# Optimization experiments

Hardware: AMD Instinct MI355X
Metric: run time of the kernel (lower is better)

Reference implementation:

```python
import jax, jax.numpy as jnp
import numpy as np

B, N, C = 4, 4096, 16
HID, OUT = 64, 64
ALL_K, K = 128, 32          # k + k_pos = 32
KD, KDP = 8, 6              # k_dilated, k_dilated_pos
EPS = 1e-5
NEG_SLOPE = 0.2


def setup_inputs() -> dict:
    ks = jax.random.split(jax.random.key(0), 12)
    C2, C4 = 2 * C, 4 * C
    return {
        "x": jax.random.normal(ks[0], (B, N, C), jnp.float32),
        "pos": jax.random.normal(ks[1], (B, N, 3), jnp.float32),
        "W1": jax.random.normal(ks[2], (C2, C2), jnp.float32) * 0.1,
        "g1": jnp.ones((C2,), jnp.float32),
        "b1": jnp.zeros((C2,), jnp.float32),
        "W2": jax.random.normal(ks[3], (HID, C4), jnp.float32) * 0.05,
        "g2": jnp.ones((HID,), jnp.float32),
        "b2": jnp.zeros((HID,), jnp.float32),
        "W3": jax.random.normal(ks[4], (OUT, HID), jnp.float32) * 0.05,
        "g3": jnp.ones((OUT,), jnp.float32),
        "b3": jnp.zeros((OUT,), jnp.float32),
    }


def pdist2(a):
    # squared pairwise distances (same top-k ordering as cdist p=2, and
    # avoids sqrt(0) on the diagonal). a: (B,N,D) -> (B,N,N)
    sq = jnp.sum(a * a, axis=-1)
    d = sq[:, :, None] + sq[:, None, :] - 2.0 * jnp.einsum('bnd,bmd->bnm', a, a)
    return jnp.maximum(d, 0.0)


def knn_excl_self(d2, k):
    # k nearest excluding self (self is the unique 0-distance nearest point)
    idx = jax.lax.top_k(-d2, k + 1)[1]
    return idx[..., 1:]


def fps(pts, npoint):
    # pts: (M, Kn, 3). Deterministic start at index 0 (torch version uses a
    # random start; only the sampled index set differs, math is identical).
    M, Kn, _ = pts.shape
    rows = jnp.arange(M)

    def body(i, state):
        centroids, distance, farthest = state
        centroids = centroids.at[:, i].set(farthest)
        centroid = pts[rows, farthest][:, None, :]            # (M,1,3)
        dist = jnp.sum((pts - centroid) ** 2, axis=-1)         # (M,Kn)
        distance = jnp.minimum(distance, dist)
        farthest = jnp.argmax(distance, axis=-1).astype(jnp.int32)
        return centroids, distance, farthest

    init = (jnp.zeros((M, npoint), jnp.int32),
            jnp.full((M, Kn), 1e10, jnp.float32),
            jnp.zeros((M,), jnp.int32))
    centroids, _, _ = jax.lax.fori_loop(0, npoint, body, init)
    return centroids


def edge_feat(feat, idx):
    # feat: (B,N,D) node features, idx: (B,N,Kn) neighbor indices
    # returns cat(neighbor - center, center): (B,N,Kn,2D)  (edge_function 249)
    nbr = feat[jnp.arange(feat.shape[0])[:, None, None], idx]  # (B,N,Kn,D)
    ctr = feat[:, :, None, :]
    return jnp.concatenate([nbr - ctr, jnp.broadcast_to(ctr, nbr.shape)], axis=-1)


def bn_lrelu(h, g, b):
    # BatchNorm2d with track_running_stats=False -> always batch stats.
    # h: (B,N,Kn,Cc), stats over (B,N,Kn) per channel.
    mu = jnp.mean(h, axis=(0, 1, 2), keepdims=True)
    var = jnp.var(h, axis=(0, 1, 2), keepdims=True)
    h = (h - mu) * jax.lax.rsqrt(var + EPS) * g + b
    return jnp.where(h > 0, h, NEG_SLOPE * h)


def reference(x, pos, W1, g1, b1, W2, g2, b2, W3, g3, b3):
    # --- dilated neighborhood: all_k nearest by position, FPS down to k ---
    cd2 = pdist2(pos)                                   # (B,N,N)
    idx_l = jax.lax.top_k(-cd2, ALL_K)[1]               # (B,N,ALL_K) incl. self
    idx_l_flat = idx_l.reshape(B * N, ALL_K)
    pts = pos.reshape(B * N, 3)[idx_l_flat]             # (B*N, ALL_K, 3)
    idx_fps_local = fps(pts, K)                         # (B*N, K)
    idx_fps = jnp.take_along_axis(idx_l_flat, idx_fps_local, axis=1)
    idx_fps = idx_fps.reshape(B, N, K)                  # (B,N,K)

    # --- dual kNN graph: k_dilated by feature distance + k_dilated_pos by pos ---
    idx_feat = knn_excl_self(pdist2(x), KD)             # (B,N,KD)
    idx_pos = knn_excl_self(cd2, KDP)                   # (B,N,KDP)
    idx1 = jnp.concatenate([idx_feat, idx_pos], axis=2)  # (B,N,KD+KDP)

    # --- conv1x1-BN-LeakyReLU on dual-graph edge features, max over nbrs ---
    e1 = edge_feat(x, idx1)                             # (B,N,14,2C)
    h1 = bn_lrelu(jnp.einsum('bnkc,oc->bnko', e1, W1), g1, b1)
    f1 = jnp.max(h1, axis=2)                            # (B,N,2C)

    # --- edge features on FPS-dilated graph, two conv1x1-BN-LeakyReLU ---
    e2 = edge_feat(f1, idx_fps)                         # (B,N,K,4C)
    h2 = bn_lrelu(jnp.einsum('bnkc,hc->bnkh', e2, W2), g2, b2)
    h3 = bn_lrelu(jnp.einsum('bnkh,oh->bnko', h2, W3), g3, b3)
    out = jnp.max(h3, axis=2)                           # (B,N,OUT)
    return out, idx1
```

## Files before the change

### kernel.cpp

```cpp
#include <hip/hip_runtime.h>

#define NPTS 4096
#define BNROWS 16384

__device__ __forceinline__ float lrelu(float h) { return h > 0.f ? h : 0.2f * h; }

__global__ __launch_bounds__(512) void knn_pos_kernel(
    const float* __restrict__ pos, int* __restrict__ idx_l,
    int* __restrict__ idx1_i, float* __restrict__ idx1_f)
{
  __shared__ unsigned long long cKey[8][512];
  __shared__ int cIdx[8][512];
  __shared__ unsigned int cCnt[8];
  int tid = threadIdx.x;
  int w = tid >> 6, lane = tid & 63;
  int r = blockIdx.x * 8 + w;
  int b = r >> 12, n = r & 4095;
  const float* pb = pos + (size_t)b * NPTS * 3;
  float cx = pb[n*3+0], cy = pb[n*3+1], cz = pb[n*3+2];
  if (lane == 0) cCnt[w] = 0u;

  unsigned int qp[32];
  int m1 = 65536, m2 = 65536, m3 = 65536;
  #pragma unroll
  for (int t = 0; t < 32; ++t) {
    unsigned int wq = 0u;
    #pragma unroll
    for (int h = 0; h < 2; ++h) {
      int j = (2*t + h) * 64 + lane;
      float dx = cx - pb[j*3+0], dy = cy - pb[j*3+1], dz = cz - pb[j*3+2];
      float d2 = dx*dx + dy*dy + dz*dz;
      int q = (int)(d2 * 1000.0f);
      q = q < 0 ? 0 : (q > 65535 ? 65535 : q);
      wq |= ((unsigned int)q) << (16*h);
      int nm1 = min(m1, q);
      int nm2 = min(m2, max(m1, q));
      int nm3 = min(m3, max(m2, q));
      m1 = nm1; m2 = nm2; m3 = nm3;
    }
    qp[t] = wq;
  }
  int lo = 0, hi = 65535;
  #pragma unroll
  for (int it = 0; it < 16; ++it) {
    int mid = (lo + hi) >> 1;
    int cnt = __popcll(__ballot(m3 <= mid));
    if (cnt >= 43) hi = mid; else lo = mid + 1;
  }
  unsigned int qt = (unsigned int)lo + 2u;

  #pragma unroll
  for (int t = 0; t < 32; ++t) {
    unsigned int wq = qp[t];
    unsigned int q0 = wq & 0xffffu, q1 = wq >> 16;
    if (q0 <= qt) { unsigned int p = atomicAdd(&cCnt[w], 1u); if (p < 512u) cIdx[w][p] = (2*t)*64 + lane; }
    if (q1 <= qt) { unsigned int p = atomicAdd(&cCnt[w], 1u); if (p < 512u) cIdx[w][p] = (2*t+1)*64 + lane; }
  }
  __syncthreads();
  unsigned int nc = cCnt[w]; if (nc > 512u) nc = 512u;

  double cxd = (double)cx, cyd = (double)cy, czd = (double)cz;
  #pragma unroll
  for (int t = 0; t < 8; ++t) {
    int c = lane + 64*t;
    unsigned long long kk = ~0ull; int id = 0x7fffffff;
    if (c < (int)nc) {
      id = cIdx[w][c];
      double dx = cxd - (double)pb[id*3+0];
      double dy = cyd - (double)pb[id*3+1];
      double dz = czd - (double)pb[id*3+2];
      kk = (unsigned long long)__double_as_longlong(dx*dx + dy*dy + dz*dz);
    }
    cKey[w][c] = kk; cIdx[w][c] = id;
  }
  __syncthreads();

  for (int k = 2; k <= 512; k <<= 1) {
    for (int j = k >> 1; j > 0; j >>= 1) {
      #pragma unroll
      for (int t = 0; t < 8; ++t) {
        int i = lane + 64*t;
        int ixj = i ^ j;
        if (ixj > i) {
          unsigned long long ka = cKey[w][i], kb = cKey[w][ixj];
          int ia = cIdx[w][i], ib = cIdx[w][ixj];
          bool agtb = (ka > kb) || (ka == kb && ia > ib);
          bool up = ((i & k) == 0);
          if (agtb == up) { cKey[w][i] = kb; cKey[w][ixj] = ka; cIdx[w][i] = ib; cIdx[w][ixj] = ia; }
        }
      }
      __syncthreads();
    }
  }
  idx_l[(size_t)r * 128 + lane]      = cIdx[w][lane];
  idx_l[(size_t)r * 128 + lane + 64] = cIdx[w][lane + 64];
  if (lane < 6) {
    int v = cIdx[w][1 + lane];
    idx1_i[r * 14 + 8 + lane] = v;
    idx1_f[r * 14 + 8 + lane] = (float)v;
  }
}

__global__ __launch_bounds__(512) void knn_feat_kernel(
    const float* __restrict__ x, int* __restrict__ idx1_i, float* __restrict__ idx1_f)
{
  __shared__ float ctrf[8][16];
  __shared__ float4 cm2[8][5];
  __shared__ unsigned short lmin[8][512];
  __shared__ int cand[8][192];
  __shared__ unsigned int cCnt[8];
  __shared__ unsigned short qtS[8];
  int tid = threadIdx.x;
  int rbase = blockIdx.x * 8;
  int b = rbase >> 12;
  const float* xb = x + (size_t)b * NPTS * 16;

  if (tid < 128) {
    int rr = tid >> 4, c = tid & 15;
    float v = xb[(size_t)((rbase + rr) & 4095) * 16 + c];
    ctrf[rr][c] = v;
    ((float*)&cm2[rr][0])[c] = -2.0f * v;
  }
  if (tid < 8) cCnt[tid] = 0u;
  __syncthreads();
  if (tid < 8) {
    float s = 0.f;
    for (int c = 0; c < 16; ++c) { float v = ctrf[tid][c]; s += v * v; }
    cm2[tid][4].x = s;
  }
  __syncthreads();

  unsigned int qp[8][4];
  int minq[8];
  #pragma unroll
  for (int r = 0; r < 8; ++r) minq[r] = 65536;

  #pragma unroll
  for (int pp = 0; pp < 4; ++pp) {
    int j0 = tid + 512 * (2*pp);
    int j1 = j0 + 512;
    const float4* xj0 = (const float4*)(xb + (size_t)j0 * 16);
    const float4* xj1 = (const float4*)(xb + (size_t)j1 * 16);
    float4 a0 = xj0[0], a1 = xj0[1], a2 = xj0[2], a3 = xj0[3];
    float4 b0 = xj1[0], b1 = xj1[1], b2 = xj1[2], b3 = xj1[3];
    float va[16] = {a0.x,a0.y,a0.z,a0.w, a1.x,a1.y,a1.z,a1.w,
                    a2.x,a2.y,a2.z,a2.w, a3.x,a3.y,a3.z,a3.w};
    float vb[16] = {b0.x,b0.y,b0.z,b0.w, b1.x,b1.y,b1.z,b1.w,
                    b2.x,b2.y,b2.z,b2.w, b3.x,b3.y,b3.z,b3.w};
    float pna = 0.f, pnb = 0.f;
    #pragma unroll
    for (int c = 0; c < 16; ++c) { pna = fmaf(va[c], va[c], pna); pnb = fmaf(vb[c], vb[c], pnb); }
    #pragma unroll
    for (int r = 0; r < 8; ++r) {
      float4 m0 = cm2[r][0], m1 = cm2[r][1], m2 = cm2[r][2], m3 = cm2[r][3];
      float c2 = cm2[r][4].x;
      float wm[16] = {m0.x,m0.y,m0.z,m0.w, m1.x,m1.y,m1.z,m1.w,
                      m2.x,m2.y,m2.z,m2.w, m3.x,m3.y,m3.z,m3.w};
      float aa = pna + c2, ab = pnb + c2;
      #pragma unroll
      for (int c = 0; c < 16; ++c) { aa = fmaf(wm[c], va[c], aa); ab = fmaf(wm[c], vb[c], ab); }
      int qa = (int)(aa * 400.0f); qa = qa < 0 ? 0 : (qa > 65535 ? 65535 : qa);
      int qb = (int)(ab * 400.0f); qb = qb < 0 ? 0 : (qb > 65535 ? 65535 : qb);
      qp[r][pp] = (unsigned int)qa | ((unsigned int)qb << 16);
      minq[r] = min(minq[r], min(qa, qb));
    }
  }
  #pragma unroll
  for (int r = 0; r < 8; ++r) lmin[r][tid] = (unsigned short)minq[r];
  __syncthreads();

  int w = tid >> 6, lane = tid & 63;
  {
    unsigned short lv[8];
    #pragma unroll
    for (int t = 0; t < 8; ++t) lv[t] = lmin[w][lane + 64*t];
    int lo = 0, hi = 65535;
    #pragma unroll
    for (int it = 0; it < 16; ++it) {
      int mid = (lo + hi) >> 1;
      int cnt = 0;
      #pragma unroll
      for (int t = 0; t < 8; ++t) cnt += __popcll(__ballot((int)lv[t] <= mid));
      if (cnt >= 10) hi = mid; else lo = mid + 1;
    }
    if (lane == 0) qtS[w] = (unsigned short)min(lo + 2, 65535);
  }
  __syncthreads();

  {
    unsigned int qts[8];
    #pragma unroll
    for (int r = 0; r < 8; ++r) qts[r] = qtS[r];
    #pragma unroll
    for (int r = 0; r < 8; ++r) {
      #pragma unroll
      for (int pp = 0; pp < 4; ++pp) {
        unsigned int wq = qp[r][pp];
        unsigned int q0 = wq & 0xffffu, q1 = wq >> 16;
        if (q0 <= qts[r]) { unsigned int p = atomicAdd(&cCnt[r], 1u); if (p < 192u) cand[r][p] = tid + 512*(2*pp); }
        if (q1 <= qts[r]) { unsigned int p = atomicAdd(&cCnt[r], 1u); if (p < 192u) cand[r][p] = tid + 512*(2*pp+1); }
      }
    }
  }
  __syncthreads();

  {
    int nc = (int)cCnt[w]; if (nc > 192) nc = 192;
    double key[3]; int kid[3];
    #pragma unroll
    for (int s = 0; s < 3; ++s) {
      int c = lane + 64*s;
      if (c < nc) {
        int id = cand[w][c];
        const float4* xp = (const float4*)(xb + (size_t)id * 16);
        float4 q0 = xp[0], q1 = xp[1], q2 = xp[2], q3 = xp[3];
        float xv[16] = {q0.x,q0.y,q0.z,q0.w, q1.x,q1.y,q1.z,q1.w,
                        q2.x,q2.y,q2.z,q2.w, q3.x,q3.y,q3.z,q3.w};
        double acc = 0.0;
        #pragma unroll
        for (int c2 = 0; c2 < 16; ++c2) { double d = (double)ctrf[w][c2] - (double)xv[c2]; acc += d * d; }
        key[s] = acc; kid[s] = id;
      } else { key[s] = 1e300; kid[s] = 0x7fffffff; }
    }
    int row = rbase + w;
    for (int it = 0; it < 9; ++it) {
      double bk = key[0]; int bi = kid[0], bs = 0;
      if (key[1] < bk || (key[1] == bk && kid[1] < bi)) { bk = key[1]; bi = kid[1]; bs = 1; }
      if (key[2] < bk || (key[2] == bk && kid[2] < bi)) { bk = key[2]; bi = kid[2]; bs = 2; }
      double rk = bk; int ri = bi;
      #pragma unroll
      for (int off = 32; off > 0; off >>= 1) {
        double ok = __shfl_xor(rk, off, 64);
        int oi = __shfl_xor(ri, off, 64);
        if (ok < rk || (ok == rk && oi < ri)) { rk = ok; ri = oi; }
      }
      if (it > 0 && lane == 0) {
        idx1_i[row * 14 + it - 1] = ri;
        idx1_f[row * 14 + it - 1] = (float)ri;
      }
      if (bi == ri) key[bs] = 1e300;
    }
  }
}

__global__ __launch_bounds__(256) void fps_kernel(
    const float* __restrict__ pos, const int* __restrict__ idx_l, int* __restrict__ idx_fps)
{
  int wave = threadIdx.x >> 6, lane = threadIdx.x & 63;
  int r = blockIdx.x * 4 + wave;
  const int* il = idx_l + (size_t)r * 128;
  int gi0 = il[lane], gi1 = il[lane + 64];
  double x0 = (double)pos[gi0*3+0], y0 = (double)pos[gi0*3+1], z0 = (double)pos[gi0*3+2];
  double x1 = (double)pos[gi1*3+0], y1 = (double)pos[gi1*3+1], z1 = (double)pos[gi1*3+2];
  double d0 = 1e10, d1 = 1e10;
  int far = 0;
  int* outp = idx_fps + (size_t)r * 32;
  for (int i = 0; i < 32; ++i) {
    int ownerLane = far & 63;
    int sel = far >> 6;
    int gsel = sel ? gi1 : gi0;
    int gout = __shfl(gsel, ownerLane, 64);
    if (lane == 0) outp[i] = gout;
    double cx = __shfl(sel ? x1 : x0, ownerLane, 64);
    double cy = __shfl(sel ? y1 : y0, ownerLane, 64);
    double cz = __shfl(sel ? z1 : z0, ownerLane, 64);
    double t0 = (x0-cx)*(x0-cx) + (y0-cy)*(y0-cy) + (z0-cz)*(z0-cz);
    double t1 = (x1-cx)*(x1-cx) + (y1-cy)*(y1-cy) + (z1-cz)*(z1-cz);
    d0 = fmin(d0, t0); d1 = fmin(d1, t1);
    double v; int p;
    if (d1 > d0) { v = d1; p = lane + 64; } else { v = d0; p = lane; }
    for (int off = 32; off > 0; off >>= 1) {
      double ov = __shfl_xor(v, off, 64);
      int op = __shfl_xor(p, off, 64);
      if (ov > v || (ov == v && op < p)) { v = ov; p = op; }
    }
    far = p;
  }
}

__global__ __launch_bounds__(256) void sv_kernel(
    const float* __restrict__ x, const float* __restrict__ W1,
    float* __restrict__ s, float* __restrict__ v)
{
  __shared__ float xs[8][16];
  __shared__ float w1t[512], w1dt[512];
  int tid = threadIdx.x;
  int rbase = blockIdx.x * 8;
  for (int i = tid; i < 512; i += 256) {
    int c = i >> 5, o = i & 31;
    float a = W1[o * 32 + c], bb = W1[o * 32 + 16 + c];
    w1t[i] = a; w1dt[i] = bb - a;
  }
  if (tid < 128) { int rr = tid >> 4, c = tid & 15; xs[rr][c] = x[(size_t)(rbase + rr) * 16 + c]; }
  __syncthreads();
  int rr = tid >> 5, o = tid & 31;
  float sa = 0.f, va = 0.f;
  #pragma unroll
  for (int c = 0; c < 16; ++c) {
    float xv = xs[rr][c];
    sa = fmaf(xv, w1t[c * 32 + o], sa);
    va = fmaf(xv, w1dt[c * 32 + o], va);
  }
  int r = rbase + rr;
  s[(size_t)r * 32 + o] = sa;
  v[(size_t)r * 32 + o] = va;
}

__global__ __launch_bounds__(256) void h1stats_kernel(
    const float* __restrict__ s, const float* __restrict__ v, const int* __restrict__ idx1_i,
    double* __restrict__ slotsH1, float* __restrict__ h1max)
{
  __shared__ int sidx[8][14];
  __shared__ float sred[256], sred2[256];
  int tid = threadIdx.x;
  int rr = tid >> 5, o = tid & 31;
  int rbase = blockIdx.x * 8;
  if (tid < 112) { int q = tid / 14, k = tid % 14; sidx[q][k] = idx1_i[(rbase + q) * 14 + k]; }
  __syncthreads();
  int r = rbase + rr;
  int broff = r & ~4095;
  float vv = v[(size_t)r * 32 + o];
  float m = -3.4e38f, ls = 0.f, lss = 0.f;
  #pragma unroll
  for (int k = 0; k < 14; ++k) {
    int j = sidx[rr][k];
    float val = s[(size_t)(broff + j) * 32 + o] + vv;
    m = fmaxf(m, val);
    ls += val; lss += val * val;
  }
  h1max[(size_t)r * 32 + o] = m;
  sred[tid] = ls; sred2[tid] = lss;
  __syncthreads();
  if (tid < 32) {
    float s2 = 0.f, ss = 0.f;
    #pragma unroll
    for (int j = 0; j < 8; ++j) { s2 += sred[j * 32 + tid]; ss += sred2[j * 32 + tid]; }
    int slot = blockIdx.x & 255;
    atomicAdd(&slotsH1[slot * 64 + tid], (double)s2);
    atomicAdd(&slotsH1[slot * 64 + 32 + tid], (double)ss);
  }
}

__global__ void finalize_stats_kernel(const double* __restrict__ slots, int C, double cnt,
    const float* __restrict__ g, const float* __restrict__ bta, float* __restrict__ scsh)
{
  int o = threadIdx.x;
  if (o < C) {
    double s = 0.0, ss = 0.0;
    for (int slot = 0; slot < 256; ++slot) { s += slots[slot * 2 * C + o]; ss += slots[slot * 2 * C + C + o]; }
    double mu = s / cnt;
    double var = ss / cnt - mu * mu;
    double rs = 1.0 / sqrt(var + 1e-5);
    float sc = (float)rs * g[o];
    float sh = bta[o] - (float)mu * sc;
    scsh[o] = sc;
    scsh[C + o] = sh;
  }
}

__global__ __launch_bounds__(256) void tu_kernel(
    const float* __restrict__ h1max, const float* __restrict__ scsh1, const float* __restrict__ W2,
    float* __restrict__ t, float* __restrict__ u)
{
  __shared__ float f1s[4][32];
  __shared__ float w2t[2048], w2dt[2048];
  int tid = threadIdx.x;
  int rbase = blockIdx.x * 4;
  for (int i = tid; i < 2048; i += 256) {
    int c = i >> 6, o = i & 63;
    float a = W2[o * 64 + c], bb = W2[o * 64 + 32 + c];
    w2t[i] = a; w2dt[i] = bb - a;
  }
  if (tid < 128) {
    int rr = tid >> 5, c = tid & 31;
    f1s[rr][c] = lrelu(h1max[(size_t)(rbase + rr) * 32 + c] * scsh1[c] + scsh1[32 + c]);
  }
  __syncthreads();
  int rr = tid >> 6, o = tid & 63;
  float ta = 0.f, ua = 0.f;
  #pragma unroll
  for (int c = 0; c < 32; ++c) {
    float fv = f1s[rr][c];
    ta = fmaf(fv, w2t[c * 64 + o], ta);
    ua = fmaf(fv, w2dt[c * 64 + o], ua);
  }
  int r = rbase + rr;
  t[(size_t)r * 64 + o] = ta;
  u[(size_t)r * 64 + o] = ua;
}

__global__ __launch_bounds__(256) void h2stats_kernel(
    const float* __restrict__ t, const float* __restrict__ u, const int* __restrict__ idx_fps,
    double* __restrict__ slotsH2)
{
  __shared__ int nids[8][32];
  __shared__ float sred[256], sred2[256];
  int tid = threadIdx.x;
  int o = tid & 63, wv = tid >> 6;
  int rbase = blockIdx.x * 8;
  { int q = tid >> 5, k = tid & 31; nids[q][k] = idx_fps[(rbase + q) * 32 + k]; }
  __syncthreads();
  float ls = 0.f, lss = 0.f;
  for (int rr = 0; rr < 8; ++rr) {
    int r = rbase + rr;
    int broff = r & ~4095;
    float uo = u[(size_t)r * 64 + o];
    #pragma unroll
    for (int i = 0; i < 8; ++i) {
      int k = wv + 4 * i;
      float val = t[(size_t)(broff + nids[rr][k]) * 64 + o] + uo;
      ls += val; lss += val * val;
    }
  }
  sred[tid] = ls; sred2[tid] = lss;
  __syncthreads();
  if (tid < 64) {
    float s2 = sred[tid] + sred[tid + 64] + sred[tid + 128] + sred[tid + 192];
    float ss = sred2[tid] + sred2[tid + 64] + sred2[tid + 128] + sred2[tid + 192];
    int slot = blockIdx.x & 255;
    atomicAdd(&slotsH2[slot * 128 + tid], (double)s2);
    atomicAdd(&slotsH2[slot * 128 + 64 + tid], (double)ss);
  }
}

#define ROWS3 8
__global__ __launch_bounds__(256, 4) void h3_kernel(
    const float* __restrict__ t, const float* __restrict__ u, const int* __restrict__ idx_fps,
    const float* __restrict__ W3, const float* __restrict__ scsh2,
    double* __restrict__ slotsH3, float* __restrict__ h3max)
{
  __shared__ float h2lds[2048];
  __shared__ float wmax[256];
  __shared__ float sred[256], sred2[256];
  __shared__ int nids[ROWS3][32];
  int tid = threadIdx.x;
  int o = tid & 63, wv = tid >> 6;
  float4 w3r[16];
  const float4* w3p = (const float4*)(W3 + o * 64);
  #pragma unroll
  for (int j = 0; j < 16; ++j) w3r[j] = w3p[j];
  float sc2o = scsh2[o], sh2o = scsh2[64 + o];
  int rbase = blockIdx.x * ROWS3;
  { int q = tid >> 5, k = tid & 31; nids[q][k] = idx_fps[(rbase + q) * 32 + k]; }
  float ls = 0.f, lss = 0.f;
  __syncthreads();
  for (int rr = 0; rr < ROWS3; ++rr) {
    int r = rbase + rr;
    int broff = r & ~4095;
    float uo = u[(size_t)r * 64 + o];
    #pragma unroll
    for (int i = 0; i < 8; ++i) {
      int k = wv + 4 * i;
      float val = t[(size_t)(broff + nids[rr][k]) * 64 + o] + uo;
      h2lds[k * 64 + o] = lrelu(val * sc2o + sh2o);
    }
    __syncthreads();
    float kmax = -3.4e38f;
    #pragma unroll
    for (int i = 0; i < 8; ++i) {
      int k = wv + 4 * i;
      const float4* hp = (const float4*)(h2lds + k * 64);
      float acc = 0.f;
      #pragma unroll
      for (int j = 0; j < 16; ++j) {
        float4 h = hp[j];
        acc = fmaf(h.x, w3r[j].x, acc); acc = fmaf(h.y, w3r[j].y, acc);
        acc = fmaf(h.z, w3r[j].z, acc); acc = fmaf(h.w, w3r[j].w, acc);
      }
      ls += acc; lss += acc * acc;
      kmax = fmaxf(kmax, acc);
    }
    wmax[tid] = kmax;
    __syncthreads();
    if (tid < 64) {
      float m = fmaxf(fmaxf(wmax[tid], wmax[64 + tid]), fmaxf(wmax[128 + tid], wmax[192 + tid]));
      h3max[(size_t)r * 64 + tid] = m;
    }
  }
  sred[tid] = ls; sred2[tid] = lss;
  __syncthreads();
  if (tid < 64) {
    float s2 = sred[tid] + sred[tid + 64] + sred[tid + 128] + sred[tid + 192];
    float ss = sred2[tid] + sred2[tid + 64] + sred2[tid + 128] + sred2[tid + 192];
    int slot = blockIdx.x & 255;
    atomicAdd(&slotsH3[slot * 128 + tid], (double)s2);
    atomicAdd(&slotsH3[slot * 128 + 64 + tid], (double)ss);
  }
}

__global__ void out_kernel(const float* __restrict__ h3max, const float* __restrict__ scsh3,
                           float* __restrict__ out)
{
  int i = blockIdx.x * 256 + threadIdx.x;
  int o = i & 63;
  out[i] = lrelu(h3max[i] * scsh3[o] + scsh3[64 + o]);
}

extern "C" void kernel_launch(void* const* d_in, const int* in_sizes, int n_in,
                              void* d_out, int out_size, void* d_ws, size_t ws_size,
                              hipStream_t stream) {
  (void)in_sizes; (void)n_in; (void)out_size; (void)ws_size;
  const float* x   = (const float*)d_in[0];
  const float* pos = (const float*)d_in[1];
  const float* W1  = (const float*)d_in[2];
  const float* g1  = (const float*)d_in[3];
  const float* b1  = (const float*)d_in[4];
  const float* W2  = (const float*)d_in[5];
  const float* g2  = (const float*)d_in[6];
  const float* b2  = (const float*)d_in[7];
  const float* W3  = (const float*)d_in[8];
  const float* g3  = (const float*)d_in[9];
  const float* b3  = (const float*)d_in[10];

  float* out      = (float*)d_out;
  float* out_idx1 = out + 1048576;

  char* ws = (char*)d_ws;
  double* slotsH1 = (double*)(ws + 0);
  double* slotsH2 = (double*)(ws + 131072);
  double* slotsH3 = (double*)(ws + 393216);
  float*  scsh1   = (float*)(ws + 655360);
  float*  scsh2   = (float*)(ws + 655616);
  float*  scsh3   = (float*)(ws + 656128);
  int*    idx_l   = (int*)(ws + 1048576);
  float*  t_buf   = (float*)(ws + 1048576);
  float*  u_buf   = (float*)(ws + 5242880);
  int*    idx_fps = (int*)(ws + 9437184);
  int*    idx1_i  = (int*)(ws + 11534336);
  float*  h1max   = (float*)(ws + 12451840);
  float*  s_buf   = (float*)(ws + 14548992);
  float*  v_buf   = (float*)(ws + 16646144);
  float*  h3max   = (float*)(ws + 18743296);

  hipMemsetAsync(d_ws, 0, 656640, stream);

  knn_pos_kernel <<<dim3(2048), dim3(512), 0, stream>>>(pos, idx_l, idx1_i, out_idx1);
  knn_feat_kernel<<<dim3(2048), dim3(512), 0, stream>>>(x, idx1_i, out_idx1);
  fps_kernel     <<<dim3(4096), dim3(256), 0, stream>>>(pos, idx_l, idx_fps);
  sv_kernel      <<<dim3(2048), dim3(256), 0, stream>>>(x, W1, s_buf, v_buf);
  h1stats_kernel <<<dim3(2048), dim3(256), 0, stream>>>(s_buf, v_buf, idx1_i, slotsH1, h1max);
  finalize_stats_kernel<<<dim3(1), dim3(64), 0, stream>>>(slotsH1, 32, 229376.0, g1, b1, scsh1);
  tu_kernel      <<<dim3(4096), dim3(256), 0, stream>>>(h1max, scsh1, W2, t_buf, u_buf);
  h2stats_kernel <<<dim3(2048), dim3(256), 0, stream>>>(t_buf, u_buf, idx_fps, slotsH2);
  finalize_stats_kernel<<<dim3(1), dim3(64), 0, stream>>>(slotsH2, 64, 524288.0, g2, b2, scsh2);
  h3_kernel      <<<dim3(2048), dim3(256), 0, stream>>>(t_buf, u_buf, idx_fps, W3, scsh2, slotsH3, h3max);
  finalize_stats_kernel<<<dim3(1), dim3(64), 0, stream>>>(slotsH3, 64, 524288.0, g3, b3, scsh3);
  out_kernel     <<<dim3(4096), dim3(256), 0, stream>>>(h3max, scsh3, out);
}
```

Baseline: 786.6 us.

## Pack kNN index into sort keys, use wave-local sync and adaptive sort size

The position-kNN kernel now packs each candidate's 12-bit index into the low bits of its double-distance key. This drops the separate index array and the tie-break comparison in the bitonic sort. Block-wide __syncthreads are replaced with an LDS waitcnt, since each wavefront owns its own candidate list, and the sort shrinks to 256 elements when few candidates survive. The costs are that distances truncated in their low mantissa bits can reorder near-ties, and correctness now relies on wave-lockstep execution for LDS visibility.

```diff
diff --git a/kernel.cpp b/kernel.cpp
--- a/kernel.cpp
+++ b/kernel.cpp
@@ -4,13 +4,14 @@
 #define BNROWS 16384
 
 __device__ __forceinline__ float lrelu(float h) { return h > 0.f ? h : 0.2f * h; }
+
+#define WSYNC asm volatile("s_waitcnt lgkmcnt(0)" ::: "memory")
 
 __global__ __launch_bounds__(512) void knn_pos_kernel(
     const float* __restrict__ pos, int* __restrict__ idx_l,
     int* __restrict__ idx1_i, float* __restrict__ idx1_f)
 {
   __shared__ unsigned long long cKey[8][512];
-  __shared__ int cIdx[8][512];
   __shared__ unsigned int cCnt[8];
   int tid = threadIdx.x;
   int w = tid >> 6, lane = tid & 63;
@@ -19,6 +20,7 @@
   const float* pb = pos + (size_t)b * NPTS * 3;
   float cx = pb[n*3+0], cy = pb[n*3+1], cz = pb[n*3+2];
   if (lane == 0) cCnt[w] = 0u;
+  WSYNC;
 
   unsigned int qp[32];
   int m1 = 65536, m2 = 65536, m3 = 65536;
@@ -53,49 +55,49 @@
   for (int t = 0; t < 32; ++t) {
     unsigned int wq = qp[t];
     unsigned int q0 = wq & 0xffffu, q1 = wq >> 16;
-    if (q0 <= qt) { unsigned int p = atomicAdd(&cCnt[w], 1u); if (p < 512u) cIdx[w][p] = (2*t)*64 + lane; }
-    if (q1 <= qt) { unsigned int p = atomicAdd(&cCnt[w], 1u); if (p < 512u) cIdx[w][p] = (2*t+1)*64 + lane; }
-  }
-  __syncthreads();
+    if (q0 <= qt) { unsigned int p = atomicAdd(&cCnt[w], 1u); if (p < 512u) cKey[w][p] = (unsigned long long)((2*t)*64 + lane); }
+    if (q1 <= qt) { unsigned int p = atomicAdd(&cCnt[w], 1u); if (p < 512u) cKey[w][p] = (unsigned long long)((2*t+1)*64 + lane); }
+  }
+  WSYNC;
   unsigned int nc = cCnt[w]; if (nc > 512u) nc = 512u;
+  int M = (nc <= 256u) ? 256 : 512;
+  int EPL = M >> 6;
 
   double cxd = (double)cx, cyd = (double)cy, czd = (double)cz;
-  #pragma unroll
-  for (int t = 0; t < 8; ++t) {
-    int c = lane + 64*t;
-    unsigned long long kk = ~0ull; int id = 0x7fffffff;
+  for (int t = 0; t < EPL; ++t) {
+    int c = lane + (t << 6);
+    unsigned long long kk = ~0ull;
     if (c < (int)nc) {
-      id = cIdx[w][c];
+      int id = (int)cKey[w][c];
       double dx = cxd - (double)pb[id*3+0];
       double dy = cyd - (double)pb[id*3+1];
       double dz = czd - (double)pb[id*3+2];
-      kk = (unsigned long long)__double_as_longlong(dx*dx + dy*dy + dz*dz);
-    }
-    cKey[w][c] = kk; cIdx[w][c] = id;
-  }
-  __syncthreads();
-
-  for (int k = 2; k <= 512; k <<= 1) {
+      double d2 = dx*dx + dy*dy + dz*dz;
+      unsigned long long bits = (unsigned long long)__double_as_longlong(d2);
+      kk = (bits & ~0xFFFull) | (unsigned long long)(unsigned int)id;
+    }
+    cKey[w][c] = kk;
+  }
+  WSYNC;
+
+  for (int k = 2; k <= M; k <<= 1) {
     for (int j = k >> 1; j > 0; j >>= 1) {
-      #pragma unroll
-      for (int t = 0; t < 8; ++t) {
-        int i = lane + 64*t;
+      for (int t = 0; t < EPL; ++t) {
+        int i = lane + (t << 6);
         int ixj = i ^ j;
         if (ixj > i) {
           unsigned long long ka = cKey[w][i], kb = cKey[w][ixj];
-          int ia = cIdx[w][i], ib = cIdx[w][ixj];
-          bool agtb = (ka > kb) || (ka == kb && ia > ib);
           bool up = ((i & k) == 0);
-          if (agtb == up) { cKey[w][i] = kb; cKey[w][ixj] = ka; cIdx[w][i] = ib; cIdx[w][ixj] = ia; }
+          if ((ka > kb) == up) { cKey[w][i] = kb; cKey[w][ixj] = ka; }
         }
       }
-      __syncthreads();
-    }
-  }
-  idx_l[(size_t)r * 128 + lane]      = cIdx[w][lane];
-  idx_l[(size_t)r * 128 + lane + 64] = cIdx[w][lane + 64];
+      WSYNC;
+    }
+  }
+  idx_l[(size_t)r * 128 + lane]      = (int)(cKey[w][lane] & 0xFFFull);
+  idx_l[(size_t)r * 128 + lane + 64] = (int)(cKey[w][lane + 64] & 0xFFFull);
   if (lane < 6) {
-    int v = cIdx[w][1 + lane];
+    int v = (int)(cKey[w][1 + lane] & 0xFFFull);
     idx1_i[r * 14 + 8 + lane] = v;
     idx1_f[r * 14 + 8 + lane] = (float)v;
   }
```

After: 654.3 us. 16.8% less time.
